# Optimization experiments

Measured on AMD Instinct MI355X. Metric: run time of the kernel, lower is better.

## Reference

```python
import jax, jax.numpy as jnp
import numpy as np

# ---- module hyperparameters (init_kwargs) ----
N = 32            # orthogonal matrix size
N_STAGES = 3      # number of scattering stages
SPARSITY = 3      # sparsity of generated FIR filters
GAIN_PER_SAMPLE = 0.9999
PULSE_SIZE = 1


def _make_shifts():
    """Faithful replica of get_random_shifts(N, sparsity_vect, pulse_size)."""
    rng = np.random.default_rng(0)
    sv = np.ones(N_STAGES)
    sv[0] = SPARSITY
    shifts = np.zeros((N_STAGES, N), dtype=np.int64)
    ps = float(PULSE_SIZE)
    for k in range(N_STAGES):
        temp = np.floor(sv[k] * (np.arange(N) + rng.random(N) * 0.99))
        shifts[k] = (temp * ps).astype(np.int64)
        ps = ps * N * sv[k]
    return shifts


def _delay_roll(V, s, row_axis):
    """shift_matrix: zero-pad the time axis so the max delay fits, then delay
    slice i along the last axis by s[i] samples (torch.roll with enough padding
    == pure delay). row_axis=0 -> 'left' (per-row), row_axis=1 -> 'right' (per-col).
    Generic inputs keep every tap occupied, so order == L-1 (matches the torch
    nonzero-based bookkeeping for random data)."""
    Nr, Nc, L = V.shape
    s = np.asarray(s).astype(np.int64)
    add = int(s.max())  # required_space.max() - L + 1 with order = L-1
    newL = L + add
    V = jnp.pad(V, ((0, 0), (0, 0), (0, add)))
    idx = (np.arange(newL)[None, :] - s[:, None]) % newL  # (N, newL) circular-roll gather
    if row_axis == 0:
        idx = jnp.broadcast_to(jnp.asarray(idx)[:, None, :], (Nr, Nc, newL))
    else:
        idx = jnp.broadcast_to(jnp.asarray(idx)[None, :, :], (Nr, Nc, newL))
    return jnp.take_along_axis(V, idx, axis=2)


def setup_inputs() -> dict:
    key = jax.random.key(0)
    U = jax.random.normal(key, (N_STAGES + 1, N, N), dtype=jnp.float32)
    shifts = jnp.asarray(_make_shifts(), dtype=jnp.int32)
    m_L = jnp.zeros((N,), dtype=jnp.int32)
    m_R = jnp.zeros((N,), dtype=jnp.int32)
    return {"U": U, "shifts": shifts, "m_L": m_L, "m_R": m_R}


def reference(U, shifts, m_L, m_R):
    # U: [K, N, N].  torch permutes to (N,N,K); V = U[:,:,0] == U[0], R stage k == U[k].
    shifts_np = np.asarray(shifts)
    K = U.shape[0]
    V = U[0][:, :, None]  # (N, N, 1) polynomial matrix
    g0 = jnp.asarray(GAIN_PER_SAMPLE, jnp.float32)
    for k in range(1, K):
        g = g0 ** shifts[k - 1].astype(jnp.float32)  # diag homogeneous attenuation
        R = U[k] * g[None, :]                        # U_k @ diag(g**shift)
        V = _delay_roll(V, shifts_np[k - 1], row_axis=0)   # left shift (per-row delay)
        # poly_matrix_conv with a length-1 polynomial R == per-tap matmul:
        # C[r,c,t] = sum_i R[r,i] * V[i,c,t]
        V = jnp.einsum('ri,ict->rct', R, V)
    V = _delay_roll(V, np.asarray(m_L), row_axis=0)  # final left shift m_{K+1}
    V = _delay_roll(V, np.asarray(m_R), row_axis=1)  # final right shift m_0
    return jnp.transpose(V, (2, 0, 1))  # (T, N, N)
```

## Files before the change

kernel.cpp:

```cpp
#include <hip/hip_runtime.h>


#define NN 32
#define LN_G -1.0000500033334732e-4f

typedef float fx4 __attribute__((ext_vector_type(4)));

__device__ __forceinline__ float tap_val(int tb, int r, int c,
                                         const float* __restrict__ sU,
                                         const int* __restrict__ inv) {
    if (tb < 0) return 0.0f;
    unsigned ut = (unsigned)tb;
    unsigned i2 = ut / 3072u;
    if (i2 >= 32u) return 0.0f;
    unsigned rem = ut - i2 * 3072u;
    unsigned i1 = rem / 96u;
    unsigned rem2 = rem - i1 * 96u;
    int i0 = inv[rem2];
    if (i0 < 0) return 0.0f;
    float gain = __expf((float)tb * LN_G);
    float f = sU[1 * NN * NN + i1 * NN + i0]
            * sU[2 * NN * NN + i2 * NN + i1]
            * sU[3 * NN * NN + r * NN + i2]
            * gain;
    return f * sU[i0 * NN + c];
}

__global__ __launch_bounds__(256) void scatter_tile_kernel(
    const float* __restrict__ U,
    const int*   __restrict__ shifts,
    const int*   __restrict__ mL,
    const int*   __restrict__ mR,
    float*       __restrict__ out,
    int T)
{
    __shared__ float sU[4 * NN * NN];
    __shared__ float sU3T[NN * NN];
    __shared__ int inv[96];
    __shared__ int smL[NN], smR[NN];
    __shared__ int sUniform, smL0, smR0;

    const int tid = threadIdx.x;
    if (tid < 96) inv[tid] = -1;
    __syncthreads();
    if (tid < NN) {
        int s1 = shifts[tid];
        if (s1 >= 0 && s1 < 96) inv[s1] = tid;
        smL[tid] = mL[tid];
        smR[tid] = mR[tid];
    }
    for (int k = tid; k < 4 * NN * NN; k += 256) sU[k] = U[k];
    for (int k = tid; k < NN * NN; k += 256) {
        sU3T[(k & 31) * NN + (k >> 5)] = U[3 * NN * NN + k];
    }
    __syncthreads();
    if (tid == 0) {
        int uL = 1, uR = 1;
        int a = smL[0], b = smR[0];
        for (int i = 1; i < NN; ++i) {
            uL &= (smL[i] == a);
            uR &= (smR[i] == b);
        }
        sUniform = uL & uR;
        smL0 = a;
        smR0 = b;
    }
    __syncthreads();

    const int wave = tid >> 6;
    const int lane = tid & 63;
    const int nwaves = gridDim.x * 4;
    const int uniform = sUniform;
    const int mL0 = smL0, mR0 = smR0;

    fx4* __restrict__ out4 = (fx4*)out;

    for (int t = blockIdx.x * 4 + wave; t < T; t += nwaves) {
        const size_t tbase = (size_t)t * 256;
        if (uniform) {
            const int tb = t - mL0 - mR0;
            int i0 = 0, i2s = 0;
            float fcom = 0.0f;
            bool tap = false;
            if (tb >= 0) {
                unsigned ut = (unsigned)tb;
                unsigned i2 = ut / 3072u;
                if (i2 < 32u) {
                    unsigned rem = ut - i2 * 3072u;
                    unsigned i1 = rem / 96u;
                    unsigned rem2 = rem - i1 * 96u;
                    int ii0 = inv[rem2];
                    if (ii0 >= 0) {
                        tap = true;
                        i0 = ii0;
                        i2s = (int)i2;
                        fcom = sU[1 * NN * NN + i1 * NN + ii0]
                             * sU[2 * NN * NN + i2 * NN + i1]
                             * __expf((float)tb * LN_G);
                    }
                }
            }
            if (tap) {
                const fx4 u0v = ((const fx4*)(sU + i0 * NN))[lane & 7];
                const int rl = lane >> 3;
#pragma unroll
                for (int j = 0; j < 4; ++j) {
                    const float u3 = sU3T[i2s * NN + j * 8 + rl];
                    const fx4 v = (fcom * u3) * u0v;
                    __builtin_nontemporal_store(v, &out4[tbase + j * 64 + lane]);
                }
            } else {
                const fx4 z = (fx4)0.0f;
#pragma unroll
                for (int j = 0; j < 4; ++j)
                    __builtin_nontemporal_store(z, &out4[tbase + j * 64 + lane]);
            }
        } else {
#pragma unroll
            for (int j = 0; j < 4; ++j) {
                const int pos4 = j * 64 + lane;
                const int r = pos4 >> 3;
                const int c = (pos4 & 7) * 4;
                const int mlr = smL[r];
                fx4 v;
                v.x = tap_val(t - mlr - smR[c + 0], r, c + 0, sU, inv);
                v.y = tap_val(t - mlr - smR[c + 1], r, c + 1, sU, inv);
                v.z = tap_val(t - mlr - smR[c + 2], r, c + 2, sU, inv);
                v.w = tap_val(t - mlr - smR[c + 3], r, c + 3, sU, inv);
                __builtin_nontemporal_store(v, &out4[tbase + pos4]);
            }
        }
    }
}

extern "C" void kernel_launch(void* const* d_in, const int* in_sizes, int n_in,
                              void* d_out, int out_size, void* d_ws, size_t ws_size,
                              hipStream_t stream) {
    const float* U      = (const float*)d_in[0];
    const int*   shifts = (const int*)d_in[1];
    const int*   mL     = (const int*)d_in[2];
    const int*   mR     = (const int*)d_in[3];
    float* out = (float*)d_out;

    const int T = out_size / (NN * NN);

    scatter_tile_kernel<<<dim3(2048), dim3(256), 0, stream>>>(
        U, shifts, mL, mR, out, T);
}
```

Baseline: 87.57 us.

## Split output into zero-fill kernel and separate nonzero-tap scatter kernel

```diff
diff --git a/kernel.cpp b/kernel.cpp
--- a/kernel.cpp
+++ b/kernel.cpp
@@ -26,7 +26,7 @@
     return f * sU[i0 * NN + c];
 }
 
-__global__ __launch_bounds__(256) void scatter_tile_kernel(
+__global__ __launch_bounds__(256) void zero_nontap_kernel(
     const float* __restrict__ U,
     const int*   __restrict__ shifts,
     const int*   __restrict__ mL,
@@ -35,87 +35,67 @@
     int T)
 {
     __shared__ float sU[4 * NN * NN];
-    __shared__ float sU3T[NN * NN];
     __shared__ int inv[96];
     __shared__ int smL[NN], smR[NN];
-    __shared__ int sUniform, smL0, smR0;
+    __shared__ unsigned smask[3];
+    __shared__ int sUniform;
 
     const int tid = threadIdx.x;
+    if (tid < 3) smask[tid] = 0u;
     if (tid < 96) inv[tid] = -1;
     __syncthreads();
     if (tid < NN) {
         int s1 = shifts[tid];
+        atomicOr(&smask[(s1 >> 5) & 3], 1u << (s1 & 31));
         if (s1 >= 0 && s1 < 96) inv[s1] = tid;
         smL[tid] = mL[tid];
         smR[tid] = mR[tid];
     }
-    for (int k = tid; k < 4 * NN * NN; k += 256) sU[k] = U[k];
-    for (int k = tid; k < NN * NN; k += 256) {
-        sU3T[(k & 31) * NN + (k >> 5)] = U[3 * NN * NN + k];
-    }
     __syncthreads();
     if (tid == 0) {
-        int uL = 1, uR = 1;
-        int a = smL[0], b = smR[0];
-        for (int i = 1; i < NN; ++i) {
-            uL &= (smL[i] == a);
-            uR &= (smR[i] == b);
-        }
+        int uL = 1, uR = 1, a = smL[0], b = smR[0];
+        for (int i = 1; i < NN; ++i) { uL &= (smL[i] == a); uR &= (smR[i] == b); }
         sUniform = uL & uR;
-        smL0 = a;
-        smR0 = b;
     }
     __syncthreads();
 
     const int wave = tid >> 6;
     const int lane = tid & 63;
-    const int nwaves = gridDim.x * 4;
-    const int uniform = sUniform;
-    const int mL0 = smL0, mR0 = smR0;
-
+    const int nw = gridDim.x * 4;
+    const int gw = blockIdx.x * 4 + wave;
     fx4* __restrict__ out4 = (fx4*)out;
 
-    for (int t = blockIdx.x * 4 + wave; t < T; t += nwaves) {
-        const size_t tbase = (size_t)t * 256;
-        if (uniform) {
-            const int tb = t - mL0 - mR0;
-            int i0 = 0, i2s = 0;
-            float fcom = 0.0f;
-            bool tap = false;
-            if (tb >= 0) {
-                unsigned ut = (unsigned)tb;
-                unsigned i2 = ut / 3072u;
-                if (i2 < 32u) {
-                    unsigned rem = ut - i2 * 3072u;
-                    unsigned i1 = rem / 96u;
-                    unsigned rem2 = rem - i1 * 96u;
-                    int ii0 = inv[rem2];
-                    if (ii0 >= 0) {
-                        tap = true;
-                        i0 = ii0;
-                        i2s = (int)i2;
-                        fcom = sU[1 * NN * NN + i1 * NN + ii0]
-                             * sU[2 * NN * NN + i2 * NN + i1]
-                             * __expf((float)tb * LN_G);
+    if (sUniform) {
+        const unsigned m0 = smask[0], m1 = smask[1], m2 = smask[2];
+        const int base = smL[0] + smR[0];
+        const fx4 z = (fx4)0.0f;
+        for (int t0 = gw * 2; t0 < T; t0 += nw * 2) {
+#pragma unroll
+            for (int u = 0; u < 2; ++u) {
+                const int t = t0 + u;
+                if (t < T) {
+                    const int tb = t - base;
+                    bool tap = false;
+                    if (tb >= 0 && tb < NN * 3072) {
+                        const unsigned rem2 = (unsigned)tb % 96u;
+                        const unsigned w = rem2 >> 5;
+                        const unsigned word = (w == 0) ? m0 : ((w == 1) ? m1 : m2);
+                        tap = (word >> (rem2 & 31u)) & 1u;
+                    }
+                    if (!tap) {
+                        const size_t tb4 = (size_t)t * 256;
+#pragma unroll
+                        for (int j = 0; j < 4; ++j)
+                            __builtin_nontemporal_store(z, &out4[tb4 + j * 64 + lane]);
                     }
                 }
             }
-            if (tap) {
-                const fx4 u0v = ((const fx4*)(sU + i0 * NN))[lane & 7];
-                const int rl = lane >> 3;
-#pragma unroll
-                for (int j = 0; j < 4; ++j) {
-                    const float u3 = sU3T[i2s * NN + j * 8 + rl];
-                    const fx4 v = (fcom * u3) * u0v;
-                    __builtin_nontemporal_store(v, &out4[tbase + j * 64 + lane]);
-                }
-            } else {
-                const fx4 z = (fx4)0.0f;
-#pragma unroll
-                for (int j = 0; j < 4; ++j)
-                    __builtin_nontemporal_store(z, &out4[tbase + j * 64 + lane]);
-            }
-        } else {
+        }
+    } else {
+        for (int k = tid; k < 4 * NN * NN; k += 256) sU[k] = U[k];
+        __syncthreads();
+        for (int t = gw; t < T; t += nw) {
+            const size_t tb4 = (size_t)t * 256;
 #pragma unroll
             for (int j = 0; j < 4; ++j) {
                 const int pos4 = j * 64 + lane;
@@ -127,7 +107,87 @@
                 v.y = tap_val(t - mlr - smR[c + 1], r, c + 1, sU, inv);
                 v.z = tap_val(t - mlr - smR[c + 2], r, c + 2, sU, inv);
                 v.w = tap_val(t - mlr - smR[c + 3], r, c + 3, sU, inv);
-                __builtin_nontemporal_store(v, &out4[tbase + pos4]);
+                __builtin_nontemporal_store(v, &out4[tb4 + pos4]);
+            }
+        }
+    }
+}
+
+__global__ __launch_bounds__(256) void tap_kernel(
+    const float* __restrict__ U,
+    const int*   __restrict__ shifts,
+    const int*   __restrict__ mL,
+    const int*   __restrict__ mR,
+    float*       __restrict__ out,
+    int T)
+{
+    __shared__ float sU0[NN * NN];
+    __shared__ float sU1[NN * NN];
+    __shared__ float sU2[NN * NN];
+    __shared__ float sU3T[NN * NN];
+    __shared__ int s1v[NN];
+    __shared__ int sUniform, sBase;
+
+    const int tid = threadIdx.x;
+    if (tid < NN) s1v[tid] = shifts[tid];
+    for (int k = tid; k < NN * NN; k += 256) {
+        sU0[k] = U[k];
+        sU1[k] = U[NN * NN + k];
+        sU2[k] = U[2 * NN * NN + k];
+        sU3T[(k & 31) * NN + (k >> 5)] = U[3 * NN * NN + k];
+    }
+    __syncthreads();
+    if (tid == 0) {
+        int uL = 1, uR = 1, a = mL[0], b = mR[0];
+        for (int i = 1; i < NN; ++i) { uL &= (mL[i] == a); uR &= (mR[i] == b); }
+        sUniform = uL & uR;
+        sBase = a + b;
+    }
+    __syncthreads();
+    if (!sUniform) return;
+
+    const int wave = tid >> 6;
+    const int lane = tid & 63;
+    const int gw = blockIdx.x * 4 + wave;
+    const int base = sBase;
+    const int rl = lane >> 3;
+    const int cb = lane & 7;
+    fx4* __restrict__ out4 = (fx4*)out;
+
+    const int c0 = gw * 4;
+    if (c0 >= NN * NN * NN) return;
+
+#pragma unroll
+    for (int p = 0; p < 2; ++p) {
+        const int cA = c0 + 2 * p, cB = cA + 1;
+        const int iA0 = cA & 31, iA1 = (cA >> 5) & 31, iA2 = cA >> 10;
+        const int iB0 = cB & 31, iB1 = (cB >> 5) & 31, iB2 = cB >> 10;
+        const int tbA = s1v[iA0] + 96 * iA1 + 3072 * iA2;
+        const int tbB = s1v[iB0] + 96 * iB1 + 3072 * iB2;
+        const int tA = tbA + base, tB = tbB + base;
+
+        const fx4 u0A = ((const fx4*)(sU0 + iA0 * NN))[cb];
+        const fx4 u0B = ((const fx4*)(sU0 + iB0 * NN))[cb];
+        const float fA = sU1[iA1 * NN + iA0] * sU2[iA2 * NN + iA1]
+                       * __expf((float)tbA * LN_G);
+        const float fB = sU1[iB1 * NN + iB0] * sU2[iB2 * NN + iB1]
+                       * __expf((float)tbB * LN_G);
+        const size_t baA = (size_t)tA * 256, baB = (size_t)tB * 256;
+
+        if (tA < T) {
+#pragma unroll
+            for (int j = 0; j < 4; ++j) {
+                const float u3 = sU3T[iA2 * NN + j * 8 + rl];
+                const fx4 v = (fA * u3) * u0A;
+                __builtin_nontemporal_store(v, &out4[baA + j * 64 + lane]);
+            }
+        }
+        if (tB < T) {
+#pragma unroll
+            for (int j = 0; j < 4; ++j) {
+                const float u3 = sU3T[iB2 * NN + j * 8 + rl];
+                const fx4 v = (fB * u3) * u0B;
+                __builtin_nontemporal_store(v, &out4[baB + j * 64 + lane]);
             }
         }
     }
@@ -144,6 +204,8 @@
 
     const int T = out_size / (NN * NN);
 
-    scatter_tile_kernel<<<dim3(2048), dim3(256), 0, stream>>>(
+    zero_nontap_kernel<<<dim3(2048), dim3(256), 0, stream>>>(
         U, shifts, mL, mR, out, T);
-}
+    tap_kernel<<<dim3(2048), dim3(256), 0, stream>>>(
+        U, shifts, mL, mR, out, T);
+}
```

Result: no change. 86.33 us (-1.4%).
